# Performance work log

Hardware: AMD Instinct MI355X
Metric: run time of the kernel (lower is better)

## Reference

```python
import jax, jax.numpy as jnp
import numpy as np

HEAD_DIM = 64  # self.head_dim, used only as the attention scale
D_MODEL = 1024


def setup_inputs() -> dict:
    key = jax.random.key(0)
    ks = jax.random.split(key, 6)
    B, S_NEW, S_CACHE, D = 4, 2048, 6144, D_MODEL
    w_scale = 1.0 / np.sqrt(D)  # keep logits well-conditioned
    return {
        "hidden_states": jax.random.normal(ks[0], (B, S_NEW, D), dtype=jnp.float32),
        "cached_key": jax.random.normal(ks[1], (B, S_CACHE, D), dtype=jnp.float32),
        "cached_value": jax.random.normal(ks[2], (B, S_CACHE, D), dtype=jnp.float32),
        "Wq": jax.random.normal(ks[3], (D, D), dtype=jnp.float32) * w_scale,
        "bq": jnp.zeros((D,), dtype=jnp.float32),
        "Wk": jax.random.normal(ks[4], (D, D), dtype=jnp.float32) * w_scale,
        "bk": jnp.zeros((D,), dtype=jnp.float32),
        "Wv": jax.random.normal(ks[5], (D, D), dtype=jnp.float32) * w_scale,
        "bv": jnp.zeros((D,), dtype=jnp.float32),
    }


def reference(hidden_states, cached_key, cached_value, Wq, bq, Wk, bk, Wv, bv):
    # Cached-branch forward: project new K/V, append to cache, full attention.
    # torch.nn.Linear: x @ W.T + b
    q = jnp.einsum("bsd,ed->bse", hidden_states, Wq) + bq          # [B, Sq, D]
    new_k = jnp.einsum("bsd,ed->bse", hidden_states, Wk) + bk      # [B, Sq, D]
    new_v = jnp.einsum("bsd,ed->bse", hidden_states, Wv) + bv
    k = jnp.concatenate([cached_key, new_k], axis=1)               # [B, Skv, D]
    v = jnp.concatenate([cached_value, new_v], axis=1)
    scale = 1.0 / jnp.sqrt(jnp.asarray(HEAD_DIM, dtype=q.dtype))
    scores = jnp.einsum("bqd,bkd->bqk", q, k) * scale              # [B, Sq, Skv]
    probs = jax.nn.softmax(scores, axis=-1)
    out = jnp.einsum("bqk,bkd->bqd", probs, v)                     # [B, Sq, D]
    return out
```

## Files before the change

kernel.cpp:

```cpp
#include <hip/hip_runtime.h>
#include <stdint.h>


#define DM 1024
#define NB 4
#define SQN 2048
#define SCC 6144
#define SKV 8192
#define NSPLIT 2
#define KSP (SKV / NSPLIT)

typedef unsigned short u16;
typedef __attribute__((ext_vector_type(8))) short short8;
typedef __attribute__((ext_vector_type(4))) float f32x4;

__device__ __forceinline__ u16 f2bf(float x) {
  unsigned u = __builtin_bit_cast(unsigned, x);
  u += 0x7fffu + ((u >> 16) & 1u);
  return (u16)(u >> 16);
}

__device__ __forceinline__ void gll16(const void* g, void* l) {
  __builtin_amdgcn_global_load_lds(
      (const __attribute__((address_space(1))) void*)g,
      (__attribute__((address_space(3))) void*)l, 16, 0, 0);
}

#define FENCE() asm volatile("" ::: "memory")
#define BARRIER()                      \
  do {                                 \
    FENCE();                           \
    __builtin_amdgcn_s_barrier();      \
    FENCE();                           \
  } while (0)

#define DSR(d, a, I) \
  asm volatile("ds_read_b128 %0, %1 offset:" #I : "=v"(d) : "v"(a))

#define LGKM(N)                                   \
  do {                                            \
    asm volatile("s_waitcnt lgkmcnt(" #N ")");    \
    __builtin_amdgcn_sched_barrier(0);            \
  } while (0)

#define MFMAQ(AF, BF, MB)                                                   \
  do {                                                                      \
    __builtin_amdgcn_s_setprio(1);                                          \
    _Pragma("unroll") for (int m = 0; m < 4; ++m)                           \
        _Pragma("unroll") for (int n = 0; n < 4; ++n) acc[(MB) + m][n] =    \
        __builtin_amdgcn_mfma_f32_16x16x32_bf16(AF[m], BF[n],               \
                                                acc[(MB) + m][n], 0, 0, 0); \
    __builtin_amdgcn_s_setprio(0);                                          \
    __builtin_amdgcn_sched_barrier(0);                                      \
  } while (0)

__global__ __launch_bounds__(256) void k_cvt(const float* __restrict__ in,
                                             u16* __restrict__ out, long n4) {
  long i = (long)blockIdx.x * 256 + threadIdx.x;
  long st = (long)gridDim.x * 256;
  for (; i < n4; i += st) {
    float4 v = ((const float4*)in)[i];
    ushort4 u;
    u.x = f2bf(v.x); u.y = f2bf(v.y); u.z = f2bf(v.z); u.w = f2bf(v.w);
    ((ushort4*)out)[i] = u;
  }
}

__global__ __launch_bounds__(256) void k_cvt_ck(const float* __restrict__ in,
                                                u16* __restrict__ out) {
  const long n4 = (long)NB * SCC * DM / 4;
  long i = (long)blockIdx.x * 256 + threadIdx.x;
  long st = (long)gridDim.x * 256;
  for (; i < n4; i += st) {
    float4 v = ((const float4*)in)[i];
    ushort4 u;
    u.x = f2bf(v.x); u.y = f2bf(v.y); u.z = f2bf(v.z); u.w = f2bf(v.w);
    long e = i * 4;
    int b = (int)(e / ((long)SCC * DM));
    long rem = e - (long)b * SCC * DM;
    *(ushort4*)(out + (long)b * SKV * DM + rem) = u;
  }
}

__global__ __launch_bounds__(256) void k_build_vt(const float* __restrict__ cv,
                                                  const u16* __restrict__ vtmp,
                                                  u16* __restrict__ VT) {
  __shared__ u16 t[64][65];
  const int kv0 = blockIdx.x * 64;
  const int d0 = blockIdx.y * 64;
  const int b = blockIdx.z;
  const int c = threadIdx.x & 63;
  const int r4 = threadIdx.x >> 6;
#pragma unroll
  for (int p = 0; p < 16; ++p) {
    int kr = p * 4 + r4;
    int kv = kv0 + kr;
    int d = d0 + c;
    u16 u;
    if (kv < SCC)
      u = f2bf(cv[((long)b * SCC + kv) * DM + d]);
    else
      u = vtmp[((long)b * SQN + (kv - SCC)) * DM + d];
    t[kr][c] = u;
  }
  __syncthreads();
#pragma unroll
  for (int p = 0; p < 16; ++p) {
    int dr = p * 4 + r4;
    VT[((long)b * DM + d0 + dr) * SKV + kv0 + c] = t[c][dr];
  }
}

template <int MODE>
__global__ __launch_bounds__(512, 2) void k_gemm8(
    const u16* __restrict__ A, const u16* __restrict__ B0,
    void* __restrict__ C0, void* __restrict__ C1, void* __restrict__ C2,
    float* __restrict__ sums, const float* __restrict__ bias0,
    const float* __restrict__ bias1, const float* __restrict__ bias2) {
  extern __shared__ char smem[];
  const int tid = threadIdx.x;
  const int lane = tid & 63;
  const int wv = tid >> 6;
  const int wr = wv >> 2;
  const int wc = wv & 3;
  const int bm = blockIdx.y * 256;
  const int bn = blockIdx.x * 256;
  const int z = blockIdx.z;

  constexpr int LD = (MODE == 2) ? SKV : DM;
  constexpr int NT = ((MODE == 2) ? KSP : DM) / 64;

  const u16 *Ab_, *Bb_;
  if constexpr (MODE == 0) {
    Ab_ = A + (long)bm * LD;
    Bb_ = B0 + (long)bn * LD;
  } else if constexpr (MODE == 1) {
    Ab_ = A + ((long)z * SKV + bm) * LD;
    Bb_ = B0 + ((long)z * SQN + bn) * LD;
  } else {
    const int bb_ = z / NSPLIT, sp = z % NSPLIT;
    Ab_ = A + ((long)bb_ * SQN + bm) * (long)SKV + (long)sp * KSP;
    Bb_ = B0 + ((long)bb_ * DM + bn) * (long)SKV + (long)sp * KSP;
  }

  const int srow = wv * 8 + (lane >> 3);
  const int scol = ((lane & 7) ^ (lane >> 3)) * 8;
  const u16* gA = Ab_ + (long)srow * LD + scol;
  const u16* gB = Bb_ + (long)srow * LD + scol;
  u16* lA = (u16*)smem + wv * 512 + lane * 8;
  u16* lB = (u16*)(smem + 65536) + wv * 512 + lane * 8;

#pragma unroll
  for (int r = 0; r < 4; ++r) gll16(gA + (long)r * 64 * LD, lA + r * 4096);
#pragma unroll
  for (int r = 0; r < 4; ++r) gll16(gB + (long)r * 64 * LD, lB + r * 4096);

  f32x4 acc[8][4];
#pragma unroll
  for (int m = 0; m < 8; ++m)
#pragma unroll
    for (int n = 0; n < 4; ++n)
#pragma unroll
      for (int j = 0; j < 4; ++j) acc[m][n][j] = 0.0f;

  const int alane = lane & 15;
  const int sw = lane & 7;
  const int s0 = lane >> 4;
  const int slot0 = ((s0 ^ sw) * 16);
  const int slot1 = (((s0 + 4) ^ sw) * 16);
  const int arow_b = (wr * 128 + alane) * 128;
  const int brow_b = (wc * 64 + alane) * 128;

  short8 Aa[4], Abf[4], Bf0[4], Bf1[4];

  for (int kt = 0; kt < NT; ++kt) {
    const int bsel = (kt & 1) * 32768;
    const int d = ((kt & 1) ^ 1) * 16384;
    const long knext = (long)((kt + 1 < NT) ? kt + 1 : kt) * 64;
    const u16* gAn = gA + knext;
    const u16* gBn = gB + knext;
    const int a0 = bsel + arow_b + slot0;
    const int a1 = bsel + arow_b + slot1;
    const int b0 = 65536 + bsel + brow_b + slot0;
    const int b1 = 65536 + bsel + brow_b + slot1;

    gll16(gAn, lA + d);
    gll16(gAn + (long)64 * LD, lA + d + 4096);
    asm volatile("s_waitcnt vmcnt(2)" ::: "memory");
    BARRIER();
    DSR(Aa[0], a0, 0); DSR(Aa[1], a0, 2048);
    DSR(Aa[2], a0, 4096); DSR(Aa[3], a0, 6144);
    DSR(Bf0[0], b0, 0); DSR(Bf0[1], b0, 2048);
    DSR(Bf0[2], b0, 4096); DSR(Bf0[3], b0, 6144);
    DSR(Abf[0], a0, 8192); DSR(Abf[1], a0, 10240);
    DSR(Abf[2], a0, 12288); DSR(Abf[3], a0, 14336);
    LGKM(4);
    MFMAQ(Aa, Bf0, 0);
    BARRIER();

    DSR(Aa[0], a1, 0); DSR(Aa[1], a1, 2048);
    DSR(Aa[2], a1, 4096); DSR(Aa[3], a1, 6144);
    DSR(Bf1[0], b1, 0); DSR(Bf1[1], b1, 2048);
    DSR(Bf1[2], b1, 4096); DSR(Bf1[3], b1, 6144);
    gll16(gAn + (long)128 * LD, lA + d + 2 * 4096);
    gll16(gAn + (long)192 * LD, lA + d + 3 * 4096);
    BARRIER();
    LGKM(8);
    MFMAQ(Abf, Bf0, 4);
    BARRIER();

    DSR(Abf[0], a1, 8192); DSR(Abf[1], a1, 10240);
    DSR(Abf[2], a1, 12288); DSR(Abf[3], a1, 14336);
    gll16(gBn, lB + d);
    gll16(gBn + (long)64 * LD, lB + d + 4096);
    BARRIER();
    LGKM(4);
    MFMAQ(Aa, Bf1, 0);
    BARRIER();

    gll16(gBn + (long)128 * LD, lB + d + 2 * 4096);
    gll16(gBn + (long)192 * LD, lB + d + 3 * 4096);
    BARRIER();
    LGKM(0);
    MFMAQ(Abf, Bf1, 4);
    BARRIER();
  }

  const int rsub = (lane >> 4) * 4;

  if constexpr (MODE == 0) {
    const int which = bm >> 10;
    const float* bp = which == 0 ? bias0 : (which == 1 ? bias1 : bias2);
    u16* Cq = (u16*)C0;
    u16* Ck = (u16*)C1;
    u16* Cv = (u16*)C2;
    const int od_base = (bm & 1023) + wr * 128 + rsub;
#pragma unroll
    for (int n = 0; n < 4; ++n) {
      int token = bn + wc * 64 + n * 16 + alane;
      u16* dst;
      if (which == 1) {
        int b = token >> 11, ss = token & 2047;
        dst = Ck + ((long)b * SKV + SCC + ss) * DM;
      } else if (which == 0) {
        dst = Cq + (long)token * DM;
      } else {
        dst = Cv + (long)token * DM;
      }
#pragma unroll
      for (int m = 0; m < 8; ++m) {
        int cc = od_base + m * 16;
        float4 bb = *(const float4*)(bp + cc);
        ushort4 u;
        u.x = f2bf(acc[m][n][0] + bb.x);
        u.y = f2bf(acc[m][n][1] + bb.y);
        u.z = f2bf(acc[m][n][2] + bb.z);
        u.w = f2bf(acc[m][n][3] + bb.w);
        *(ushort4*)(dst + cc) = u;
      }
    }
  } else if constexpr (MODE == 1) {
    u16* Pp = (u16*)C0 + (long)z * SQN * SKV;
    float* sb = sums + z * SQN;
    const float CE = 0.18033688011112042f;
    const int kv_base = bm + wr * 128 + rsub;
#pragma unroll
    for (int n = 0; n < 4; ++n) {
      int q = bn + wc * 64 + n * 16 + alane;
      u16* prow = Pp + (long)q * SKV;
      float part = 0.f;
#pragma unroll
      for (int m = 0; m < 8; ++m) {
        int kv = kv_base + m * 16;
        float e0 = exp2f(acc[m][n][0] * CE);
        float e1 = exp2f(acc[m][n][1] * CE);
        float e2 = exp2f(acc[m][n][2] * CE);
        float e3 = exp2f(acc[m][n][3] * CE);
        part += (e0 + e1) + (e2 + e3);
        ushort4 u;
        u.x = f2bf(e0); u.y = f2bf(e1); u.z = f2bf(e2); u.w = f2bf(e3);
        *(ushort4*)(prow + kv) = u;
      }
      part += __shfl_xor(part, 16);
      part += __shfl_xor(part, 32);
      if ((lane >> 4) == 0) atomicAdd(&sb[q], part);
    }
  } else {
    float* Cp = (float*)C0 + (long)z * SQN * DM;
#pragma unroll
    for (int n = 0; n < 4; ++n) {
      int col = bn + wc * 64 + n * 16 + alane;
#pragma unroll
      for (int m = 0; m < 8; ++m)
#pragma unroll
        for (int j = 0; j < 4; ++j) {
          int row = bm + wr * 128 + m * 16 + rsub + j;
          Cp[(long)row * DM + col] = acc[m][n][j];
        }
    }
  }
}

__global__ __launch_bounds__(256) void k_reduce(const float* __restrict__ Op,
                                                const float* __restrict__ sums,
                                                float* __restrict__ out) {
  const long n4 = (long)NB * SQN * DM / 4;
  long i = (long)blockIdx.x * 256 + threadIdx.x;
  if (i >= n4) return;
  long e = i * 4;
  int b = (int)(e / ((long)SQN * DM));
  long rem = e - (long)b * SQN * DM;
  int row = (int)(rem / DM);
  const long z4 = (long)SQN * DM / 4;
  long i0 = (long)(b * NSPLIT) * z4 + (rem >> 2);
  float4 a0 = ((const float4*)Op)[i0];
  float4 a1 = ((const float4*)Op)[i0 + z4];
  float inv = 1.0f / sums[b * SQN + row];
  float4 r;
  r.x = (a0.x + a1.x) * inv;
  r.y = (a0.y + a1.y) * inv;
  r.z = (a0.z + a1.z) * inv;
  r.w = (a0.w + a1.w) * inv;
  ((float4*)out)[i] = r;
}

extern "C" void kernel_launch(void* const* d_in, const int* in_sizes, int n_in,
                              void* d_out, int out_size, void* d_ws, size_t ws_size,
                              hipStream_t stream) {
  const float* hidden = (const float*)d_in[0];
  const float* ck = (const float*)d_in[1];
  const float* cv = (const float*)d_in[2];
  const float* Wq = (const float*)d_in[3];
  const float* bq = (const float*)d_in[4];
  const float* Wk = (const float*)d_in[5];
  const float* bk = (const float*)d_in[6];
  const float* Wv = (const float*)d_in[7];
  const float* bv = (const float*)d_in[8];
  (void)in_sizes; (void)n_in; (void)out_size; (void)ws_size;

  hipFuncSetAttribute(reinterpret_cast<const void*>(&k_gemm8<0>),
                      hipFuncAttributeMaxDynamicSharedMemorySize, 131072);
  hipFuncSetAttribute(reinterpret_cast<const void*>(&k_gemm8<1>),
                      hipFuncAttributeMaxDynamicSharedMemorySize, 131072);
  hipFuncSetAttribute(reinterpret_cast<const void*>(&k_gemm8<2>),
                      hipFuncAttributeMaxDynamicSharedMemorySize, 131072);

  char* base = (char*)d_ws;
  size_t off = 0;
  auto alloc = [&](size_t bytes) {
    char* p = base + off;
    off = (off + bytes + 255) & ~(size_t)255;
    return p;
  };
  u16* Hb = (u16*)alloc((size_t)NB * SQN * DM * 2);
  u16* Wall = (u16*)alloc((size_t)3 * DM * DM * 2);
  u16* Qb = (u16*)alloc((size_t)NB * SQN * DM * 2);
  u16* Kb = (u16*)alloc((size_t)NB * SKV * DM * 2);
  u16* Vtmp = (u16*)alloc((size_t)NB * SQN * DM * 2);
  float* Opart = (float*)base;
  size_t opart_bytes = (size_t)NB * NSPLIT * SQN * DM * 4;
  if (off < opart_bytes) off = (opart_bytes + 255) & ~(size_t)255;
  u16* VT = (u16*)alloc((size_t)NB * DM * SKV * 2);
  u16* P = (u16*)alloc((size_t)NB * SQN * SKV * 2);
  float* sums = (float*)alloc((size_t)NB * SQN * 4);

  k_cvt<<<2048, 256, 0, stream>>>(hidden, Hb, (long)NB * SQN * DM / 4);
  k_cvt<<<512, 256, 0, stream>>>(Wq, Wall, (long)DM * DM / 4);
  k_cvt<<<512, 256, 0, stream>>>(Wk, Wall + (size_t)DM * DM, (long)DM * DM / 4);
  k_cvt<<<512, 256, 0, stream>>>(Wv, Wall + (size_t)2 * DM * DM, (long)DM * DM / 4);
  k_cvt_ck<<<4096, 256, 0, stream>>>(ck, Kb);

  k_gemm8<0><<<dim3(32, 12, 1), 512, 131072, stream>>>(
      Wall, Hb, Qb, Kb, Vtmp, nullptr, bq, bk, bv);

  k_build_vt<<<dim3(SKV / 64, DM / 64, NB), 256, 0, stream>>>(cv, Vtmp, VT);

  hipMemsetAsync(sums, 0, (size_t)NB * SQN * 4, stream);
  k_gemm8<1><<<dim3(SQN / 256, SKV / 256, NB), 512, 131072, stream>>>(
      Kb, Qb, P, nullptr, nullptr, sums, nullptr, nullptr, nullptr);

  k_gemm8<2><<<dim3(DM / 256, SQN / 256, NB * NSPLIT), 512, 131072, stream>>>(
      P, VT, Opart, nullptr, nullptr, nullptr, nullptr, nullptr, nullptr);

  k_reduce<<<(NB * SQN * DM / 4 + 255) / 256, 256, 0, stream>>>(
      Opart, sums, (float*)d_out);
}
```

Before: 471.3 us.

## Restructure GEMM mainloop into quadrant-based 4-phase schedule with half-tile prefetch

Rewrites the shared GEMM kernel's main loop. Each wave now computes its output as four quadrants (M-half by N-half), and the global-to-LDS prefetch of the next k-tile is split into matching half-tiles interleaved with those quadrants. Waits use fixed vmcnt(4) and lgkmcnt(0), and the loop is unrolled by two with constant buffer indices. The aim is to overlap loads with MFMA work more evenly and simplify LDS addressing. In exchange it changes the wave-to-tile mapping and the barrier and wait placement, so correctness depends on the new waits being sufficient.

```diff
diff --git a/kernel.cpp b/kernel.cpp
--- a/kernel.cpp
+++ b/kernel.cpp
@@ -35,23 +35,13 @@
   } while (0)
 
 #define DSR(d, a, I) \
-  asm volatile("ds_read_b128 %0, %1 offset:" #I : "=v"(d) : "v"(a))
-
-#define LGKM(N)                                   \
-  do {                                            \
-    asm volatile("s_waitcnt lgkmcnt(" #N ")");    \
-    __builtin_amdgcn_sched_barrier(0);            \
-  } while (0)
-
-#define MFMAQ(AF, BF, MB)                                                   \
-  do {                                                                      \
-    __builtin_amdgcn_s_setprio(1);                                          \
-    _Pragma("unroll") for (int m = 0; m < 4; ++m)                           \
-        _Pragma("unroll") for (int n = 0; n < 4; ++n) acc[(MB) + m][n] =    \
-        __builtin_amdgcn_mfma_f32_16x16x32_bf16(AF[m], BF[n],               \
-                                                acc[(MB) + m][n], 0, 0, 0); \
-    __builtin_amdgcn_s_setprio(0);                                          \
-    __builtin_amdgcn_sched_barrier(0);                                      \
+  asm volatile("ds_read_b128 %0, %1 offset:%2" : "=v"(d) : "v"(a), "i"(I))
+
+#define VMC4() asm volatile("s_waitcnt vmcnt(4)" ::: "memory")
+#define LGKM0()                                    \
+  do {                                             \
+    asm volatile("s_waitcnt lgkmcnt(0)" ::: "memory"); \
+    __builtin_amdgcn_sched_barrier(0);             \
   } while (0)
 
 __global__ __launch_bounds__(256) void k_cvt(const float* __restrict__ in,
@@ -143,17 +133,37 @@
     Bb_ = B0 + ((long)bb_ * DM + bn) * (long)SKV + (long)sp * KSP;
   }
 
-  const int srow = wv * 8 + (lane >> 3);
-  const int scol = ((lane & 7) ^ (lane >> 3)) * 8;
-  const u16* gA = Ab_ + (long)srow * LD + scol;
-  const u16* gB = Bb_ + (long)srow * LD + scol;
-  u16* lA = (u16*)smem + wv * 512 + lane * 8;
-  u16* lB = (u16*)(smem + 65536) + wv * 512 + lane * 8;
-
-#pragma unroll
-  for (int r = 0; r < 4; ++r) gll16(gA + (long)r * 64 * LD, lA + r * 4096);
-#pragma unroll
-  for (int r = 0; r < 4; ++r) gll16(gB + (long)r * 64 * LD, lB + r * 4096);
+  const int sg = tid >> 3;
+  const int ssl = ((tid & 7) ^ (sg & 7)) * 8;
+  const u16* gA[2][2];
+  const u16* gB[2][2];
+#pragma unroll
+  for (int mh = 0; mh < 2; ++mh)
+#pragma unroll
+    for (int g = 0; g < 2; ++g) {
+      gA[mh][g] = Ab_ + (long)(g * 128 + mh * 64 + sg) * LD + ssl;
+      gB[mh][g] = Bb_ + (long)((g * 2 + (sg >> 5)) * 64 + mh * 32 + (sg & 31)) * LD + ssl;
+    }
+  u16* lA = (u16*)smem + tid * 8;
+  u16* lB = (u16*)smem + 32768 + tid * 8;
+
+#define SA(MH, BUFN, KO)                                              \
+  do {                                                                \
+    gll16(gA[MH][0] + (KO), lA + (BUFN)*16384 + (MH)*8192);           \
+    gll16(gA[MH][1] + (KO), lA + (BUFN)*16384 + (MH)*8192 + 4096);    \
+  } while (0)
+#define SB(NH, BUFN, KO)                                              \
+  do {                                                                \
+    gll16(gB[NH][0] + (KO), lB + (BUFN)*16384 + (NH)*8192);           \
+    gll16(gB[NH][1] + (KO), lB + (BUFN)*16384 + (NH)*8192 + 4096);    \
+  } while (0)
+
+  SA(0, 0, 0);
+  SB(0, 0, 0);
+  SB(1, 0, 0);
+  SA(1, 0, 0);
+  VMC4();
+  BARRIER();
 
   f32x4 acc[8][4];
 #pragma unroll
@@ -168,63 +178,81 @@
   const int s0 = lane >> 4;
   const int slot0 = ((s0 ^ sw) * 16);
   const int slot1 = (((s0 + 4) ^ sw) * 16);
-  const int arow_b = (wr * 128 + alane) * 128;
-  const int brow_b = (wc * 64 + alane) * 128;
-
-  short8 Aa[4], Abf[4], Bf0[4], Bf1[4];
-
-  for (int kt = 0; kt < NT; ++kt) {
-    const int bsel = (kt & 1) * 32768;
-    const int d = ((kt & 1) ^ 1) * 16384;
-    const long knext = (long)((kt + 1 < NT) ? kt + 1 : kt) * 64;
-    const u16* gAn = gA + knext;
-    const u16* gBn = gB + knext;
-    const int a0 = bsel + arow_b + slot0;
-    const int a1 = bsel + arow_b + slot1;
-    const int b0 = 65536 + bsel + brow_b + slot0;
-    const int b1 = 65536 + bsel + brow_b + slot1;
-
-    gll16(gAn, lA + d);
-    gll16(gAn + (long)64 * LD, lA + d + 4096);
-    asm volatile("s_waitcnt vmcnt(2)" ::: "memory");
-    BARRIER();
-    DSR(Aa[0], a0, 0); DSR(Aa[1], a0, 2048);
-    DSR(Aa[2], a0, 4096); DSR(Aa[3], a0, 6144);
-    DSR(Bf0[0], b0, 0); DSR(Bf0[1], b0, 2048);
-    DSR(Bf0[2], b0, 4096); DSR(Bf0[3], b0, 6144);
-    DSR(Abf[0], a0, 8192); DSR(Abf[1], a0, 10240);
-    DSR(Abf[2], a0, 12288); DSR(Abf[3], a0, 14336);
-    LGKM(4);
-    MFMAQ(Aa, Bf0, 0);
-    BARRIER();
-
-    DSR(Aa[0], a1, 0); DSR(Aa[1], a1, 2048);
-    DSR(Aa[2], a1, 4096); DSR(Aa[3], a1, 6144);
-    DSR(Bf1[0], b1, 0); DSR(Bf1[1], b1, 2048);
-    DSR(Bf1[2], b1, 4096); DSR(Bf1[3], b1, 6144);
-    gll16(gAn + (long)128 * LD, lA + d + 2 * 4096);
-    gll16(gAn + (long)192 * LD, lA + d + 3 * 4096);
-    BARRIER();
-    LGKM(8);
-    MFMAQ(Abf, Bf0, 4);
-    BARRIER();
-
-    DSR(Abf[0], a1, 8192); DSR(Abf[1], a1, 10240);
-    DSR(Abf[2], a1, 12288); DSR(Abf[3], a1, 14336);
-    gll16(gBn, lB + d);
-    gll16(gBn + (long)64 * LD, lB + d + 4096);
-    BARRIER();
-    LGKM(4);
-    MFMAQ(Aa, Bf1, 0);
-    BARRIER();
-
-    gll16(gBn + (long)128 * LD, lB + d + 2 * 4096);
-    gll16(gBn + (long)192 * LD, lB + d + 3 * 4096);
-    BARRIER();
-    LGKM(0);
-    MFMAQ(Abf, Bf1, 4);
-    BARRIER();
-  }
+  const int aBase = (wr * 64 + alane) * 128;
+  const int bBase = (wc * 32 + alane) * 128;
+
+  short8 aF[4][2];
+  short8 bF[2][2][2];
+
+#define ARD8(MH, AR0, AR1)                          \
+  _Pragma("unroll") for (int ms = 0; ms < 4; ++ms) { \
+    DSR(aF[ms][0], AR0, (MH)*16384 + ms * 2048);     \
+    DSR(aF[ms][1], AR1, (MH)*16384 + ms * 2048);     \
+  }
+#define BRD4(NH, BR0, BR1)                          \
+  _Pragma("unroll") for (int ns = 0; ns < 2; ++ns) { \
+    DSR(bF[NH][ns][0], BR0, (NH)*16384 + ns * 2048); \
+    DSR(bF[NH][ns][1], BR1, (NH)*16384 + ns * 2048); \
+  }
+#define MFMA_Q(MH, NH)                                                     \
+  do {                                                                     \
+    __builtin_amdgcn_s_setprio(1);                                         \
+    _Pragma("unroll") for (int ms = 0; ms < 4; ++ms)                       \
+    _Pragma("unroll") for (int ns = 0; ns < 2; ++ns)                       \
+    _Pragma("unroll") for (int kk = 0; kk < 2; ++kk)                       \
+        acc[(MH)*4 + ms][(NH)*2 + ns] =                                    \
+            __builtin_amdgcn_mfma_f32_16x16x32_bf16(                       \
+                aF[ms][kk], bF[NH][ns][kk], acc[(MH)*4 + ms][(NH)*2 + ns], \
+                0, 0, 0);                                                  \
+    __builtin_amdgcn_s_setprio(0);                                         \
+    __builtin_amdgcn_sched_barrier(0);                                     \
+  } while (0)
+
+#define TILE_BODY(BUF, KT)                                            \
+  do {                                                                \
+    const long ko = (long)(((KT) + 1 < NT) ? (KT) + 1 : (KT)) * 64;   \
+    const int aR0 = (BUF)*32768 + aBase + slot0;                      \
+    const int aR1 = (BUF)*32768 + aBase + slot1;                      \
+    const int bR0 = 65536 + (BUF)*32768 + bBase + slot0;              \
+    const int bR1 = 65536 + (BUF)*32768 + bBase + slot1;              \
+                                                  \
+    ARD8(0, aR0, aR1);                                                \
+    BRD4(0, bR0, bR1);                                                \
+    SA(0, (BUF) ^ 1, ko);                                             \
+    VMC4();                                                           \
+    BARRIER();                                                        \
+    LGKM0();                                                          \
+    MFMA_Q(0, 0);                                                     \
+                                                  \
+    BRD4(1, bR0, bR1);                                                \
+    SB(0, (BUF) ^ 1, ko);                                             \
+    VMC4();                                                           \
+    BARRIER();                                                        \
+    LGKM0();                                                          \
+    MFMA_Q(0, 1);                                                     \
+                                                  \
+    ARD8(1, aR0, aR1);                                                \
+    SB(1, (BUF) ^ 1, ko);                                             \
+    BARRIER();                                                        \
+    LGKM0();                                                          \
+    MFMA_Q(1, 1);                                                     \
+                                 \
+    SA(1, (BUF) ^ 1, ko);                                             \
+    VMC4();                                                           \
+    BARRIER();                                                        \
+    MFMA_Q(1, 0);                                                     \
+  } while (0)
+
+  for (int t2 = 0; t2 < NT; t2 += 2) {
+    TILE_BODY(0, t2);
+    TILE_BODY(1, t2 + 1);
+  }
+#undef TILE_BODY
+#undef ARD8
+#undef BRD4
+#undef MFMA_Q
+#undef SA
+#undef SB
 
   const int rsub = (lane >> 4) * 4;
 
```

Result: faster. 439.2 us (-6.8%).
